# Kernel tuning notes

Hardware: AMD Instinct MI355X
Metric: run time of the kernel (lower is better)

Reference implementation:

```python
import jax, jax.numpy as jnp
import numpy as np

ALPHA = 0.2          # LeakyReLU negative slope
NEG_INF = -9e15      # mask value from the torch code
B, N, F, E, H, S, T, L = 32, 128, 78, 12, 256, 20, 13, 3


def setup_inputs() -> dict:
    key = jax.random.key(0)
    ks = jax.random.split(key, 20)
    sc = 0.05  # param scale
    inp = {
        "node_features": jax.random.normal(ks[0], (B, N, F), jnp.float32),
        "edge_features": jax.random.normal(ks[1], (B, N, N, E), jnp.float32),
        "adj_matrix": jax.random.randint(ks[2], (B, N, N), 0, 2).astype(jnp.int32),
        "scaffold_features": jax.random.normal(ks[3], (B, S), jnp.float32),
        # node projection (Linear F->H, with bias)
        "W_node": jax.random.normal(ks[4], (F, H), jnp.float32) * sc,
        "b_node": jnp.zeros((H,), jnp.float32),
        # stacked GAT layer params: W (H->H, no bias), a (2H->1, no bias)
        "gat_W": jax.random.normal(ks[5], (L, H, H), jnp.float32) * sc,
        "gat_a": jax.random.normal(ks[6], (L, 2 * H), jnp.float32) * sc,
        # scaffold projection (S->H)
        "W_sc": jax.random.normal(ks[7], (S, H), jnp.float32) * sc,
        "b_sc": jnp.zeros((H,), jnp.float32),
        # graph_pooling MLP: H -> H/2 -> H/4 (shared for graph + scaffold paths)
        "gp_w1": jax.random.normal(ks[8], (H, H // 2), jnp.float32) * sc,
        "gp_b1": jnp.zeros((H // 2,), jnp.float32),
        "gp_w2": jax.random.normal(ks[9], (H // 2, H // 4), jnp.float32) * sc,
        "gp_b2": jnp.zeros((H // 4,), jnp.float32),
        # output MLP: (H/4 + H/4) -> H/2 -> T
        "out_w1": jax.random.normal(ks[10], (H // 2, H // 2), jnp.float32) * sc,
        "out_b1": jnp.zeros((H // 2,), jnp.float32),
        "out_w2": jax.random.normal(ks[11], (H // 2, T), jnp.float32) * sc,
        "out_b2": jnp.zeros((T,), jnp.float32),
    }
    return inp


def _gat_stack(x, adj_matrix, gat_W, gat_a):
    # x: (B,N,H); adj: (B,N,N) int
    mask = adj_matrix > 0
    n_layers, _, h_dim = gat_W.shape
    for l in range(n_layers):
        h = jnp.einsum("bnf,fh->bnh", x, gat_W[l])      # (B,N,H)
        a1, a2 = gat_a[l, :h_dim], gat_a[l, h_dim:]
        # a . [h_i ; h_j] == h_i.a1 + h_j.a2 (exact decomposition of the
        # O(N^2, 2H) concat in the torch code)
        s1 = h @ a1                                       # (B,N)
        s2 = h @ a2                                       # (B,N)
        e = jax.nn.leaky_relu(s1[:, :, None] + s2[:, None, :], ALPHA)
        att = jnp.where(mask, e, NEG_INF)                 # (B,N,N)
        att = jax.nn.softmax(att, axis=-1)
        h_prime = jnp.einsum("bij,bjh->bih", att, h)
        x = jax.nn.relu(h_prime)                          # relu after layer (dropout = identity, eval)
    return x


def _pool(z, gp_w1, gp_b1, gp_w2, gp_b2):
    z = jax.nn.relu(z @ gp_w1 + gp_b1)
    return jax.nn.relu(z @ gp_w2 + gp_b2)


def reference(node_features, edge_features, adj_matrix, scaffold_features,
              W_node, b_node, gat_W, gat_a, W_sc, b_sc,
              gp_w1, gp_b1, gp_w2, gp_b2, out_w1, out_b1, out_w2, out_b2):
    # edge_features is accepted but unused in the original forward
    x = node_features @ W_node + b_node                  # (B,N,H)
    x = _gat_stack(x, adj_matrix, gat_W, gat_a)
    graph = x.mean(axis=1)                               # (B,H)
    g = _pool(graph, gp_w1, gp_b1, gp_w2, gp_b2)         # (B,H/4)
    s = _pool(scaffold_features @ W_sc + b_sc, gp_w1, gp_b1, gp_w2, gp_b2)
    c = jnp.concatenate([g, s], axis=-1)                 # (B,H/2)
    hdn = jax.nn.relu(c @ out_w1 + out_b1)
    return hdn @ out_w2 + out_b2                         # (B,T)
```

## Files before the change

### kernel.cpp

```cpp
#include <hip/hip_runtime.h>
#include <hip/hip_bf16.h>

#define NEG_INF -9.0e15f

using u16 = unsigned short;

__device__ __forceinline__ float b2f(__hip_bfloat16 v) { return __bfloat162float(v); }
__device__ __forceinline__ float ldv(const float* p, int i) { return p[i]; }
__device__ __forceinline__ float ldv(const __hip_bfloat16* p, int i) { return __bfloat162float(p[i]); }

__device__ __forceinline__ void async16(const void* g, void* l) {
    __builtin_amdgcn_global_load_lds(
        (__attribute__((address_space(1))) void*)(g),
        (__attribute__((address_space(3))) void*)(l), 16, 0, 0);
}

__device__ __forceinline__ int sniff(const void* wnode) {
    const u16* w = (const u16*)wnode;
    int lane = threadIdx.x & 63;
    u16 u = w[2 * lane];
    int e = (u >> 7) & 0xFF;
    unsigned long long m = __ballot(e >= 100 && e <= 140);
    return __popcll(m) >= 48;
}


template <int IS_BF>
__device__ __forceinline__ void gat_core(
    char* smem, int t, int row0, int pb0,
    const void* __restrict__ gat_W, const void* __restrict__ gat_a, int l,
    float* __restrict__ hw, float* __restrict__ s1w, float* __restrict__ s2w) {
    float* xsT = (float*)smem;
    const int tx = t & 63, w = t >> 6;
    const int c0 = 4 * tx;
    float acc0[4], acc1[4];
    #pragma unroll
    for (int j = 0; j < 4; ++j) { acc0[j] = 0.f; acc1[j] = 0.f; }

    if (IS_BF) {
        u16* Wb0 = (u16*)(smem + 10240);
        const u16* Wl = (const u16*)gat_W + (size_t)l * 65536;
        auto stage_rows = [&](int r0, int nr, int buf) {
            const char* g = (const char*)Wl + (size_t)r0 * 512;
            char* lp = (char*)(Wb0 + buf * 8192);
            int bytes = nr * 512;
            for (int off = t * 16; off < bytes; off += 4096)
                async16(g + off, lp + off);
        };
        int pb = pb0;
        for (int tt = 0; tt < 8; ++tt) {
            if (tt < 7) stage_rows(32 * (tt + 1), 32, pb ^ 1);
            const u16* Wp = Wb0 + pb * 8192;
            const int k0 = 32 * tt;
            #pragma unroll 8
            for (int kk = 0; kk < 32; ++kk) {
                uint2 wv = *(const uint2*)(Wp + kk * 256 + c0);
                float w0 = __uint_as_float(wv.x << 16);
                float w1 = __uint_as_float(wv.x & 0xffff0000u);
                float w2 = __uint_as_float(wv.y << 16);
                float w3 = __uint_as_float(wv.y & 0xffff0000u);
                float2 xp = *(const float2*)&xsT[(k0 + kk) * 10 + 2 * w];
                acc0[0] += xp.x * w0; acc0[1] += xp.x * w1;
                acc0[2] += xp.x * w2; acc0[3] += xp.x * w3;
                acc1[0] += xp.y * w0; acc1[1] += xp.y * w1;
                acc1[2] += xp.y * w2; acc1[3] += xp.y * w3;
            }
            __syncthreads();
            pb ^= 1;
        }
        const __hip_bfloat16* ga = (const __hip_bfloat16*)gat_a + (size_t)l * 512;
        float d10 = 0.f, d20 = 0.f, d11 = 0.f, d21 = 0.f;
        #pragma unroll
        for (int j = 0; j < 4; ++j) {
            float a1v = b2f(ga[c0 + j]), a2v = b2f(ga[256 + c0 + j]);
            d10 += acc0[j] * a1v; d20 += acc0[j] * a2v;
            d11 += acc1[j] * a1v; d21 += acc1[j] * a2v;
        }
        #pragma unroll
        for (int off = 1; off < 64; off <<= 1) {
            d10 += __shfl_xor(d10, off, 64); d20 += __shfl_xor(d20, off, 64);
            d11 += __shfl_xor(d11, off, 64); d21 += __shfl_xor(d21, off, 64);
        }
        if (tx == 0) {
            s1w[row0 + 2 * w] = d10;     s2w[row0 + 2 * w] = d20;
            s1w[row0 + 2 * w + 1] = d11; s2w[row0 + 2 * w + 1] = d21;
        }
        *(float4*)&hw[(size_t)(row0 + 2 * w) * 256 + c0]     = (float4){acc0[0], acc0[1], acc0[2], acc0[3]};
        *(float4*)&hw[(size_t)(row0 + 2 * w + 1) * 256 + c0] = (float4){acc1[0], acc1[1], acc1[2], acc1[3]};
    } else {
        const float* Wlf = (const float*)gat_W + (size_t)l * 65536;
        const float* gaf = (const float*)gat_a + (size_t)l * 512;
        #pragma unroll 4
        for (int k = 0; k < 256; ++k) {
            float4 wf = *(const float4*)(Wlf + k * 256 + c0);
            float2 xp = *(const float2*)&xsT[k * 10 + 2 * w];
            acc0[0] += xp.x * wf.x; acc0[1] += xp.x * wf.y;
            acc0[2] += xp.x * wf.z; acc0[3] += xp.x * wf.w;
            acc1[0] += xp.y * wf.x; acc1[1] += xp.y * wf.y;
            acc1[2] += xp.y * wf.z; acc1[3] += xp.y * wf.w;
        }
        float d10 = 0.f, d20 = 0.f, d11 = 0.f, d21 = 0.f;
        #pragma unroll
        for (int j = 0; j < 4; ++j) {
            float a1v = gaf[c0 + j], a2v = gaf[256 + c0 + j];
            d10 += acc0[j] * a1v; d20 += acc0[j] * a2v;
            d11 += acc1[j] * a1v; d21 += acc1[j] * a2v;
        }
        #pragma unroll
        for (int off = 1; off < 64; off <<= 1) {
            d10 += __shfl_xor(d10, off, 64); d20 += __shfl_xor(d20, off, 64);
            d11 += __shfl_xor(d11, off, 64); d21 += __shfl_xor(d21, off, 64);
        }
        if (tx == 0) {
            s1w[row0 + 2 * w] = d10;     s2w[row0 + 2 * w] = d20;
            s1w[row0 + 2 * w + 1] = d11; s2w[row0 + 2 * w + 1] = d21;
        }
        *(float4*)&hw[(size_t)(row0 + 2 * w) * 256 + c0]     = (float4){acc0[0], acc0[1], acc0[2], acc0[3]};
        *(float4*)&hw[(size_t)(row0 + 2 * w + 1) * 256 + c0] = (float4){acc1[0], acc1[1], acc1[2], acc1[3]};
    }
}

__device__ __forceinline__ void attn_compute(
    char* smem, int t, int b, int s,
    const float* __restrict__ hw, const float* __restrict__ s1w,
    const float* __restrict__ s2w, const int* __restrict__ adj,
    float ac0[4], float ac1[4]) {
    float (*att_t)[10] = (float (*)[10])smem;
    float* hbuf = (float*)(smem + 5120);
    const int i0 = s << 3;
    const int w = t >> 6, lane = t & 63;
    const char* hbytes = (const char*)(hw + (size_t)b * 32768);
    const int ph = s & 3;
    {
        char* lb = (char*)hbuf;
        const char* g = hbytes + ph * 32768;
        #pragma unroll
        for (int i = 0; i < 8; ++i)
            async16(g + i * 4096 + t * 16, lb + i * 4096 + t * 16);
    }
    {
        int cc0 = lane, cc1 = lane + 64;
        int ir0 = i0 + 2 * w, ir1 = ir0 + 1;
        const int* a0 = adj + (size_t)(b * 128 + ir0) * 128;
        const int* a1 = adj + (size_t)(b * 128 + ir1) * 128;
        int m00 = a0[cc0], m01 = a0[cc1], m10 = a1[cc0], m11 = a1[cc1];
        float sv0 = s1w[b * 128 + ir0], sv1 = s1w[b * 128 + ir1];
        float t0 = s2w[b * 128 + cc0],  t1 = s2w[b * 128 + cc1];
        float e00 = sv0 + t0; e00 = (e00 >= 0.f) ? e00 : 0.2f * e00;
        float e01 = sv0 + t1; e01 = (e01 >= 0.f) ? e01 : 0.2f * e01;
        float e10 = sv1 + t0; e10 = (e10 >= 0.f) ? e10 : 0.2f * e10;
        float e11 = sv1 + t1; e11 = (e11 >= 0.f) ? e11 : 0.2f * e11;
        float v00 = (m00 > 0) ? e00 : NEG_INF;
        float v01 = (m01 > 0) ? e01 : NEG_INF;
        float v10 = (m10 > 0) ? e10 : NEG_INF;
        float v11 = (m11 > 0) ? e11 : NEG_INF;
        float mx0 = fmaxf(v00, v01), mx1 = fmaxf(v10, v11);
        #pragma unroll
        for (int off = 1; off < 64; off <<= 1) {
            mx0 = fmaxf(mx0, __shfl_xor(mx0, off, 64));
            mx1 = fmaxf(mx1, __shfl_xor(mx1, off, 64));
        }
        float p00 = __expf(v00 - mx0), p01 = __expf(v01 - mx0);
        float p10 = __expf(v10 - mx1), p11 = __expf(v11 - mx1);
        float sm0 = p00 + p01, sm1 = p10 + p11;
        #pragma unroll
        for (int off = 1; off < 64; off <<= 1) {
            sm0 += __shfl_xor(sm0, off, 64);
            sm1 += __shfl_xor(sm1, off, 64);
        }
        float inv0 = 1.0f / sm0, inv1 = 1.0f / sm1;
        att_t[cc0][2 * w]     = p00 * inv0;
        att_t[cc1][2 * w]     = p01 * inv0;
        att_t[cc0][2 * w + 1] = p10 * inv1;
        att_t[cc1][2 * w + 1] = p11 * inv1;
    }
    __syncthreads();
    int tx = t & 63, ty = t >> 6;
    #pragma unroll
    for (int j = 0; j < 4; ++j) { ac0[j] = 0.f; ac1[j] = 0.f; }
    for (int c = 0; c < 4; ++c) {
        if (c < 3) {
            char* lb = (char*)hbuf + ((c + 1) & 1) * 32768;
            const char* g = hbytes + (((c + 1 + ph) & 3) * 32768);
            #pragma unroll
            for (int i = 0; i < 8; ++i)
                async16(g + i * 4096 + t * 16, lb + i * 4096 + t * 16);
        }
        const float* hc = hbuf + (c & 1) * 8192;
        const int jb = ((c + ph) & 3) * 32;
        #pragma unroll 4
        for (int jj = 0; jj < 32; ++jj) {
            float4 hv = *(const float4*)&hc[jj * 256 + 4 * tx];
            float2 ap = *(const float2*)&att_t[jb + jj][2 * ty];
            ac0[0] += ap.x * hv.x; ac0[1] += ap.x * hv.y;
            ac0[2] += ap.x * hv.z; ac0[3] += ap.x * hv.w;
            ac1[0] += ap.y * hv.x; ac1[1] += ap.y * hv.y;
            ac1[2] += ap.y * hv.z; ac1[3] += ap.y * hv.w;
        }
        __syncthreads();
    }
}

__global__ __launch_bounds__(256) void k_gat_first(
    const void* __restrict__ nf, const void* __restrict__ Wn_raw,
    const void* __restrict__ bn,
    const void* __restrict__ gat_W, const void* __restrict__ gat_a,
    float* __restrict__ hw, float* __restrict__ s1w, float* __restrict__ s2w) {
    __shared__ __align__(16) char smem[43008];
    const int t = threadIdx.x;
    const int row0 = blockIdx.x * 8;
    const int tx = t & 63, w = t >> 6;
    const int c0 = 4 * tx;
    float* xsT = (float*)smem;
    float acc0[4], acc1[4];

    if (sniff(Wn_raw)) {
        u16* Wb0 = (u16*)(smem + 10240);
        const u16* Wl = (const u16*)gat_W;
        auto stage = [&](const u16* src, int r0, int nr, int buf) {
            const char* g = (const char*)src + (size_t)r0 * 512;
            char* lp = (char*)(Wb0 + buf * 8192);
            int bytes = nr * 512;
            for (int off = t * 16; off < bytes; off += 4096)
                async16(g + off, lp + off);
        };
        auto tile = [&](int buf, int k0, int nr) {
            const u16* Wp = Wb0 + buf * 8192;
            #pragma unroll 8
            for (int kk = 0; kk < nr; ++kk) {
                uint2 wv = *(const uint2*)(Wp + kk * 256 + c0);
                float w0 = __uint_as_float(wv.x << 16);
                float w1 = __uint_as_float(wv.x & 0xffff0000u);
                float w2 = __uint_as_float(wv.y << 16);
                float w3 = __uint_as_float(wv.y & 0xffff0000u);
                float2 xp = *(const float2*)&xsT[(k0 + kk) * 10 + 2 * w];
                acc0[0] += xp.x * w0; acc0[1] += xp.x * w1;
                acc0[2] += xp.x * w2; acc0[3] += xp.x * w3;
                acc1[0] += xp.y * w0; acc1[1] += xp.y * w1;
                acc1[2] += xp.y * w2; acc1[3] += xp.y * w3;
            }
        };
        const u16* Wnl = (const u16*)Wn_raw;
        stage(Wnl, 0, 32, 0);
        const u16* nfu = (const u16*)nf;
        for (int i = t; i < 624; i += 256) {
            int r = i / 78, k = i - r * 78;
            xsT[k * 10 + r] = __uint_as_float(((unsigned)nfu[(row0 + r) * 78 + k]) << 16);
        }
        const __hip_bfloat16* bnb = (const __hip_bfloat16*)bn;
        #pragma unroll
        for (int j = 0; j < 4; ++j) { acc0[j] = b2f(bnb[c0 + j]); acc1[j] = acc0[j]; }
        __syncthreads();
        stage(Wnl, 32, 32, 1);
        tile(0, 0, 32);
        __syncthreads();
        stage(Wnl, 64, 14, 0);
        tile(1, 32, 32);
        __syncthreads();
        stage(Wl, 0, 32, 1);
        tile(0, 64, 14);
        __syncthreads();
        #pragma unroll
        for (int j = 0; j < 4; ++j) {
            xsT[(c0 + j) * 10 + 2 * w]     = acc0[j];
            xsT[(c0 + j) * 10 + 2 * w + 1] = acc1[j];
        }
        __syncthreads();
        gat_core<1>(smem, t, row0, 1, gat_W, gat_a, 0, hw, s1w, s2w);
    } else {
        const float* nff = (const float*)nf;
        for (int i = t; i < 624; i += 256) {
            int r = i / 78, k = i - r * 78;
            xsT[k * 10 + r] = nff[(row0 + r) * 78 + k];
        }
        __syncthreads();
        const float* Wnf = (const float*)Wn_raw;
        const float* bnf = (const float*)bn;
        #pragma unroll
        for (int j = 0; j < 4; ++j) { acc0[j] = bnf[c0 + j]; acc1[j] = acc0[j]; }
        for (int k = 0; k < 78; ++k) {
            float4 wf = *(const float4*)(Wnf + k * 256 + c0);
            float2 xp = *(const float2*)&xsT[k * 10 + 2 * w];
            acc0[0] += xp.x * wf.x; acc0[1] += xp.x * wf.y;
            acc0[2] += xp.x * wf.z; acc0[3] += xp.x * wf.w;
            acc1[0] += xp.y * wf.x; acc1[1] += xp.y * wf.y;
            acc1[2] += xp.y * wf.z; acc1[3] += xp.y * wf.w;
        }
        __syncthreads();
        #pragma unroll
        for (int j = 0; j < 4; ++j) {
            xsT[(c0 + j) * 10 + 2 * w]     = acc0[j];
            xsT[(c0 + j) * 10 + 2 * w + 1] = acc1[j];
        }
        __syncthreads();
        gat_core<0>(smem, t, row0, 0, gat_W, gat_a, 0, hw, s1w, s2w);
    }
}

__global__ __launch_bounds__(256) void k_attn_gat(
    const float* __restrict__ h_in, const float* __restrict__ s1_in,
    const float* __restrict__ s2_in, const int* __restrict__ adj,
    const void* __restrict__ gat_W, const void* __restrict__ gat_a, int l,
    const void* __restrict__ Wn_raw,
    float* __restrict__ h_out, float* __restrict__ s1_out, float* __restrict__ s2_out) {
    __shared__ __align__(16) char smem[74752];
    const int t = threadIdx.x;
    const int blk = blockIdx.x;
    const int b = blk >> 4, s = blk & 15;
    const int row0 = blk * 8;
    const int isbf = sniff(Wn_raw);

    float ac0[4], ac1[4];
    attn_compute(smem, t, b, s, h_in, s1_in, s2_in, adj, ac0, ac1);
    const int tx = t & 63, ty = t >> 6;
    const int c0 = 4 * tx;
    float* xsT = (float*)smem;
    if (isbf) {
        u16* Wb0 = (u16*)(smem + 10240);
        const u16* Wl = (const u16*)gat_W + (size_t)l * 65536;
        for (int off = t * 16; off < 16384; off += 4096)
            async16((const char*)Wl + off, (char*)Wb0 + off);
    }
    #pragma unroll
    for (int j = 0; j < 4; ++j) {
        xsT[(c0 + j) * 10 + 2 * ty]     = fmaxf(ac0[j], 0.f);
        xsT[(c0 + j) * 10 + 2 * ty + 1] = fmaxf(ac1[j], 0.f);
    }
    __syncthreads();
    if (isbf)
        gat_core<1>(smem, t, row0, 0, gat_W, gat_a, l, h_out, s1_out, s2_out);
    else
        gat_core<0>(smem, t, row0, 0, gat_W, gat_a, l, h_out, s1_out, s2_out);
}

__global__ __launch_bounds__(256) void k_attn_pool(
    const float* __restrict__ h_in, const float* __restrict__ s1_in,
    const float* __restrict__ s2_in, const int* __restrict__ adj,
    float* __restrict__ gpart) {
    __shared__ __align__(16) char smem[74752];
    const int t = threadIdx.x;
    const int blk = blockIdx.x;
    const int b = blk >> 4, s = blk & 15;
    float ac0[4], ac1[4];
    attn_compute(smem, t, b, s, h_in, s1_in, s2_in, adj, ac0, ac1);
    float (*pool_red)[256] = (float (*)[256])(smem + 70656);
    const int tx = t & 63, ty = t >> 6;
    float4 pr = {(fmaxf(ac0[0],0.f) + fmaxf(ac1[0],0.f)) * (1.f/128.f),
                 (fmaxf(ac0[1],0.f) + fmaxf(ac1[1],0.f)) * (1.f/128.f),
                 (fmaxf(ac0[2],0.f) + fmaxf(ac1[2],0.f)) * (1.f/128.f),
                 (fmaxf(ac0[3],0.f) + fmaxf(ac1[3],0.f)) * (1.f/128.f)};
    *(float4*)&pool_red[ty][4 * tx] = pr;
    __syncthreads();
    if (t < 64) {
        float4 r0 = ((const float4*)&pool_red[0][0])[t];
        float4 r1 = ((const float4*)&pool_red[1][0])[t];
        float4 r2 = ((const float4*)&pool_red[2][0])[t];
        float4 r3 = ((const float4*)&pool_red[3][0])[t];
        float4 o = {r0.x+r1.x+r2.x+r3.x, r0.y+r1.y+r2.y+r3.y,
                    r0.z+r1.z+r2.z+r3.z, r0.w+r1.w+r2.w+r3.w};
        *(float4*)&gpart[((size_t)b * 16 + s) * 256 + 4 * t] = o;
    }
}

template <typename T>
__device__ __forceinline__ void head_body(
    int b, int t, const float* __restrict__ gpart,
    const T* scaf, const T* W_sc, const T* b_sc,
    const T* gp_w1, const T* gp_b1, const T* gp_w2, const T* gp_b2,
    const T* out_w1, const T* out_b1, const T* out_w2, const T* out_b2,
    float* gin_s, float* sproj, float* scaf_s,
    float* red1, float* red2, float* z1g, float* z1s,
    float* cvec, float* hdn, float* outv) {
    float g = 0.f;
    #pragma unroll
    for (int gg = 0; gg < 16; ++gg) g += gpart[((size_t)b * 16 + gg) * 256 + t];
    gin_s[t] = g;
    if (t < 20) scaf_s[t] = ldv(scaf, b * 20 + t);
    __syncthreads();
    {
        float sa = ldv(b_sc, t);
        #pragma unroll
        for (int k = 0; k < 20; ++k) sa += scaf_s[k] * ldv(W_sc, k * 256 + t);
        sproj[t] = sa;
    }
    __syncthreads();
    {
        int j = t & 127, khalf = t >> 7;
        int k0 = khalf * 128;
        float a1 = 0.f, a2 = 0.f;
        #pragma unroll 16
        for (int kk = 0; kk < 128; ++kk) {
            int k = k0 + kk;
            float wv = ldv(gp_w1, k * 128 + j);
            a1 += gin_s[k] * wv;
            a2 += sproj[k] * wv;
        }
        red1[t] = a1; red2[t] = a2;
    }
    __syncthreads();
    if (t < 128) {
        float bb = ldv(gp_b1, t);
        z1g[t] = fmaxf(bb + red1[t] + red1[t + 128], 0.f);
        z1s[t] = fmaxf(bb + red2[t] + red2[t + 128], 0.f);
    }
    __syncthreads();
    {
        int j = t & 63, q = t >> 6;
        int k0 = q * 32;
        float a1 = 0.f, a2 = 0.f;
        #pragma unroll
        for (int kk = 0; kk < 32; ++kk) {
            int k = k0 + kk;
            float wv = ldv(gp_w2, k * 64 + j);
            a1 += z1g[k] * wv;
            a2 += z1s[k] * wv;
        }
        red1[t] = a1; red2[t] = a2;
    }
    __syncthreads();
    if (t < 64) {
        float bb = ldv(gp_b2, t);
        cvec[t]      = fmaxf(bb + red1[t] + red1[t + 64] + red1[t + 128] + red1[t + 192], 0.f);
        cvec[64 + t] = fmaxf(bb + red2[t] + red2[t + 64] + red2[t + 128] + red2[t + 192], 0.f);
    }
    __syncthreads();
    {
        int j = t & 127, khalf = t >> 7;
        int k0 = khalf * 64;
        float a = 0.f;
        #pragma unroll 16
        for (int kk = 0; kk < 64; ++kk) {
            int k = k0 + kk;
            a += cvec[k] * ldv(out_w1, k * 128 + j);
        }
        red1[t] = a;
    }
    __syncthreads();
    if (t < 128) hdn[t] = fmaxf(ldv(out_b1, t) + red1[t] + red1[t + 128], 0.f);
    __syncthreads();
    if (t < 13) {
        float a = ldv(out_b2, t);
        #pragma unroll 16
        for (int k = 0; k < 128; ++k) a += hdn[k] * ldv(out_w2, k * 13 + t);
        outv[t] = a;
    }
}

__global__ __launch_bounds__(256) void k_head(
    const float* __restrict__ gpart, const void* __restrict__ scaf,
    const void* __restrict__ W_sc, const void* __restrict__ b_sc,
    const void* __restrict__ gp_w1, const void* __restrict__ gp_b1,
    const void* __restrict__ gp_w2, const void* __restrict__ gp_b2,
    const void* __restrict__ out_w1, const void* __restrict__ out_b1,
    const void* __restrict__ out_w2, const void* __restrict__ out_b2,
    void* __restrict__ out, const void* __restrict__ Wn) {
    int isbf = sniff(Wn);
    int b = blockIdx.x;
    int t = threadIdx.x;
    __shared__ float gin_s[256], sproj[256], scaf_s[20];
    __shared__ float red1[256], red2[256];
    __shared__ float z1g[128], z1s[128], cvec[128], hdn[128], outv[13];
    if (isbf) {
        head_body<__hip_bfloat16>(b, t, gpart,
            (const __hip_bfloat16*)scaf, (const __hip_bfloat16*)W_sc, (const __hip_bfloat16*)b_sc,
            (const __hip_bfloat16*)gp_w1, (const __hip_bfloat16*)gp_b1,
            (const __hip_bfloat16*)gp_w2, (const __hip_bfloat16*)gp_b2,
            (const __hip_bfloat16*)out_w1, (const __hip_bfloat16*)out_b1,
            (const __hip_bfloat16*)out_w2, (const __hip_bfloat16*)out_b2,
            gin_s, sproj, scaf_s, red1, red2, z1g, z1s, cvec, hdn, outv);
    } else {
        head_body<float>(b, t, gpart,
            (const float*)scaf, (const float*)W_sc, (const float*)b_sc,
            (const float*)gp_w1, (const float*)gp_b1,
            (const float*)gp_w2, (const float*)gp_b2,
            (const float*)out_w1, (const float*)out_b1,
            (const float*)out_w2, (const float*)out_b2,
            gin_s, sproj, scaf_s, red1, red2, z1g, z1s, cvec, hdn, outv);
    }
    __syncthreads();
    if (t < 13) {
        if (isbf) ((__hip_bfloat16*)out)[b * 13 + t] = __float2bfloat16(outv[t]);
        else      ((float*)out)[b * 13 + t] = outv[t];
    }
}

extern "C" void kernel_launch(void* const* d_in, const int* in_sizes, int n_in,
                              void* d_out, int out_size, void* d_ws, size_t ws_size,
                              hipStream_t stream) {
    (void)in_sizes; (void)n_in; (void)out_size; (void)ws_size;
    const void* nf     = d_in[0];
    const int*  adj    = (const int*)d_in[2];
    const void* scaf   = d_in[3];
    const void* W_node = d_in[4];
    const void* b_node = d_in[5];
    const void* gat_W  = d_in[6];
    const void* gat_a  = d_in[7];
    const void* W_sc   = d_in[8];
    const void* b_sc   = d_in[9];
    const void* gp_w1  = d_in[10];
    const void* gp_b1  = d_in[11];
    const void* gp_w2  = d_in[12];
    const void* gp_b2  = d_in[13];
    const void* out_w1 = d_in[14];
    const void* out_b1 = d_in[15];
    const void* out_w2 = d_in[16];
    const void* out_b2 = d_in[17];

    float* ws    = (float*)d_ws;
    float* hA    = ws;
    float* hB    = ws + 1048576;
    float* s1A   = ws + 2097152;
    float* s2A   = ws + 2101248;
    float* s1B   = ws + 2105344;
    float* s2B   = ws + 2109440;
    float* gpart = ws + 2113536;

    k_gat_first<<<512, 256, 0, stream>>>(nf, W_node, b_node, gat_W, gat_a,
                                         hA, s1A, s2A);
    k_attn_gat<<<512, 256, 0, stream>>>(hA, s1A, s2A, adj, gat_W, gat_a, 1,
                                        W_node, hB, s1B, s2B);
    k_attn_gat<<<512, 256, 0, stream>>>(hB, s1B, s2B, adj, gat_W, gat_a, 2,
                                        W_node, hA, s1A, s2A);
    k_attn_pool<<<512, 256, 0, stream>>>(hA, s1A, s2A, adj, gpart);
    k_head<<<32, 256, 0, stream>>>(gpart, scaf, W_sc, b_sc, gp_w1, gp_b1, gp_w2, gp_b2,
                                   out_w1, out_b1, out_w2, out_b2, d_out, W_node);
}
```

Measured before the change: 205.0 us.

## Halve rows per block to double grid size and raise occupancy

Each block now handles 4 node rows instead of 8, one per wave, so every kernel launches 1024 blocks instead of 512. Shared memory per block roughly halves, and launch bounds request 4 blocks per CU, aiming for better latency hiding and fuller use of the CUs. The trade-off is that each block reloads the full weight matrix and the per-graph h tiles for half as many rows, which doubles that global and LDS traffic per useful output. The head kernel now reduces 32 partial sums per graph instead of 16.

```diff
diff --git a/kernel.cpp b/kernel.cpp
--- a/kernel.cpp
+++ b/kernel.cpp
@@ -33,16 +33,14 @@
     float* xsT = (float*)smem;
     const int tx = t & 63, w = t >> 6;
     const int c0 = 4 * tx;
-    float acc0[4], acc1[4];
-    #pragma unroll
-    for (int j = 0; j < 4; ++j) { acc0[j] = 0.f; acc1[j] = 0.f; }
+    float acc[4] = {0.f, 0.f, 0.f, 0.f};
 
     if (IS_BF) {
-        u16* Wb0 = (u16*)(smem + 10240);
+        u16* Wb0 = (u16*)(smem + 5120);
         const u16* Wl = (const u16*)gat_W + (size_t)l * 65536;
         auto stage_rows = [&](int r0, int nr, int buf) {
             const char* g = (const char*)Wl + (size_t)r0 * 512;
-            char* lp = (char*)(Wb0 + buf * 8192);
+            char* lp = (char*)Wb0 + buf * 16384;
             int bytes = nr * 512;
             for (int off = t * 16; off < bytes; off += 4096)
                 async16(g + off, lp + off);
@@ -59,64 +57,50 @@
                 float w1 = __uint_as_float(wv.x & 0xffff0000u);
                 float w2 = __uint_as_float(wv.y << 16);
                 float w3 = __uint_as_float(wv.y & 0xffff0000u);
-                float2 xp = *(const float2*)&xsT[(k0 + kk) * 10 + 2 * w];
-                acc0[0] += xp.x * w0; acc0[1] += xp.x * w1;
-                acc0[2] += xp.x * w2; acc0[3] += xp.x * w3;
-                acc1[0] += xp.y * w0; acc1[1] += xp.y * w1;
-                acc1[2] += xp.y * w2; acc1[3] += xp.y * w3;
+                float xv = xsT[(k0 + kk) * 5 + w];
+                acc[0] += xv * w0; acc[1] += xv * w1;
+                acc[2] += xv * w2; acc[3] += xv * w3;
             }
             __syncthreads();
             pb ^= 1;
         }
         const __hip_bfloat16* ga = (const __hip_bfloat16*)gat_a + (size_t)l * 512;
-        float d10 = 0.f, d20 = 0.f, d11 = 0.f, d21 = 0.f;
+        float d1 = 0.f, d2 = 0.f;
         #pragma unroll
         for (int j = 0; j < 4; ++j) {
-            float a1v = b2f(ga[c0 + j]), a2v = b2f(ga[256 + c0 + j]);
-            d10 += acc0[j] * a1v; d20 += acc0[j] * a2v;
-            d11 += acc1[j] * a1v; d21 += acc1[j] * a2v;
+            d1 += acc[j] * b2f(ga[c0 + j]);
+            d2 += acc[j] * b2f(ga[256 + c0 + j]);
         }
         #pragma unroll
         for (int off = 1; off < 64; off <<= 1) {
-            d10 += __shfl_xor(d10, off, 64); d20 += __shfl_xor(d20, off, 64);
-            d11 += __shfl_xor(d11, off, 64); d21 += __shfl_xor(d21, off, 64);
-        }
-        if (tx == 0) {
-            s1w[row0 + 2 * w] = d10;     s2w[row0 + 2 * w] = d20;
-            s1w[row0 + 2 * w + 1] = d11; s2w[row0 + 2 * w + 1] = d21;
-        }
-        *(float4*)&hw[(size_t)(row0 + 2 * w) * 256 + c0]     = (float4){acc0[0], acc0[1], acc0[2], acc0[3]};
-        *(float4*)&hw[(size_t)(row0 + 2 * w + 1) * 256 + c0] = (float4){acc1[0], acc1[1], acc1[2], acc1[3]};
+            d1 += __shfl_xor(d1, off, 64);
+            d2 += __shfl_xor(d2, off, 64);
+        }
+        if (tx == 0) { s1w[row0 + w] = d1; s2w[row0 + w] = d2; }
+        *(float4*)&hw[(size_t)(row0 + w) * 256 + c0] = (float4){acc[0], acc[1], acc[2], acc[3]};
     } else {
         const float* Wlf = (const float*)gat_W + (size_t)l * 65536;
         const float* gaf = (const float*)gat_a + (size_t)l * 512;
         #pragma unroll 4
         for (int k = 0; k < 256; ++k) {
             float4 wf = *(const float4*)(Wlf + k * 256 + c0);
-            float2 xp = *(const float2*)&xsT[k * 10 + 2 * w];
-            acc0[0] += xp.x * wf.x; acc0[1] += xp.x * wf.y;
-            acc0[2] += xp.x * wf.z; acc0[3] += xp.x * wf.w;
-            acc1[0] += xp.y * wf.x; acc1[1] += xp.y * wf.y;
-            acc1[2] += xp.y * wf.z; acc1[3] += xp.y * wf.w;
-        }
-        float d10 = 0.f, d20 = 0.f, d11 = 0.f, d21 = 0.f;
+            float xv = xsT[k * 5 + w];
+            acc[0] += xv * wf.x; acc[1] += xv * wf.y;
+            acc[2] += xv * wf.z; acc[3] += xv * wf.w;
+        }
+        float d1 = 0.f, d2 = 0.f;
         #pragma unroll
         for (int j = 0; j < 4; ++j) {
-            float a1v = gaf[c0 + j], a2v = gaf[256 + c0 + j];
-            d10 += acc0[j] * a1v; d20 += acc0[j] * a2v;
-            d11 += acc1[j] * a1v; d21 += acc1[j] * a2v;
+            d1 += acc[j] * gaf[c0 + j];
+            d2 += acc[j] * gaf[256 + c0 + j];
         }
         #pragma unroll
         for (int off = 1; off < 64; off <<= 1) {
-            d10 += __shfl_xor(d10, off, 64); d20 += __shfl_xor(d20, off, 64);
-            d11 += __shfl_xor(d11, off, 64); d21 += __shfl_xor(d21, off, 64);
-        }
-        if (tx == 0) {
-            s1w[row0 + 2 * w] = d10;     s2w[row0 + 2 * w] = d20;
-            s1w[row0 + 2 * w + 1] = d11; s2w[row0 + 2 * w + 1] = d21;
-        }
-        *(float4*)&hw[(size_t)(row0 + 2 * w) * 256 + c0]     = (float4){acc0[0], acc0[1], acc0[2], acc0[3]};
-        *(float4*)&hw[(size_t)(row0 + 2 * w + 1) * 256 + c0] = (float4){acc1[0], acc1[1], acc1[2], acc1[3]};
+            d1 += __shfl_xor(d1, off, 64);
+            d2 += __shfl_xor(d2, off, 64);
+        }
+        if (tx == 0) { s1w[row0 + w] = d1; s2w[row0 + w] = d2; }
+        *(float4*)&hw[(size_t)(row0 + w) * 256 + c0] = (float4){acc[0], acc[1], acc[2], acc[3]};
     }
 }
 
@@ -124,102 +108,88 @@
     char* smem, int t, int b, int s,
     const float* __restrict__ hw, const float* __restrict__ s1w,
     const float* __restrict__ s2w, const int* __restrict__ adj,
-    float ac0[4], float ac1[4]) {
-    float (*att_t)[10] = (float (*)[10])smem;
-    float* hbuf = (float*)(smem + 5120);
-    const int i0 = s << 3;
+    float ac[4]) {
+    float (*att_t)[6] = (float (*)[6])smem;
+    float* hbuf = (float*)(smem + 3072);
+    const int i0 = s << 2;
     const int w = t >> 6, lane = t & 63;
     const char* hbytes = (const char*)(hw + (size_t)b * 32768);
-    const int ph = s & 3;
+    const int ph = s & 7;
     {
         char* lb = (char*)hbuf;
-        const char* g = hbytes + ph * 32768;
-        #pragma unroll
-        for (int i = 0; i < 8; ++i)
+        const char* g = hbytes + ph * 16384;
+        #pragma unroll
+        for (int i = 0; i < 4; ++i)
             async16(g + i * 4096 + t * 16, lb + i * 4096 + t * 16);
     }
     {
         int cc0 = lane, cc1 = lane + 64;
-        int ir0 = i0 + 2 * w, ir1 = ir0 + 1;
-        const int* a0 = adj + (size_t)(b * 128 + ir0) * 128;
-        const int* a1 = adj + (size_t)(b * 128 + ir1) * 128;
-        int m00 = a0[cc0], m01 = a0[cc1], m10 = a1[cc0], m11 = a1[cc1];
-        float sv0 = s1w[b * 128 + ir0], sv1 = s1w[b * 128 + ir1];
-        float t0 = s2w[b * 128 + cc0],  t1 = s2w[b * 128 + cc1];
-        float e00 = sv0 + t0; e00 = (e00 >= 0.f) ? e00 : 0.2f * e00;
-        float e01 = sv0 + t1; e01 = (e01 >= 0.f) ? e01 : 0.2f * e01;
-        float e10 = sv1 + t0; e10 = (e10 >= 0.f) ? e10 : 0.2f * e10;
-        float e11 = sv1 + t1; e11 = (e11 >= 0.f) ? e11 : 0.2f * e11;
-        float v00 = (m00 > 0) ? e00 : NEG_INF;
-        float v01 = (m01 > 0) ? e01 : NEG_INF;
-        float v10 = (m10 > 0) ? e10 : NEG_INF;
-        float v11 = (m11 > 0) ? e11 : NEG_INF;
-        float mx0 = fmaxf(v00, v01), mx1 = fmaxf(v10, v11);
-        #pragma unroll
-        for (int off = 1; off < 64; off <<= 1) {
-            mx0 = fmaxf(mx0, __shfl_xor(mx0, off, 64));
-            mx1 = fmaxf(mx1, __shfl_xor(mx1, off, 64));
-        }
-        float p00 = __expf(v00 - mx0), p01 = __expf(v01 - mx0);
-        float p10 = __expf(v10 - mx1), p11 = __expf(v11 - mx1);
-        float sm0 = p00 + p01, sm1 = p10 + p11;
-        #pragma unroll
-        for (int off = 1; off < 64; off <<= 1) {
-            sm0 += __shfl_xor(sm0, off, 64);
-            sm1 += __shfl_xor(sm1, off, 64);
-        }
-        float inv0 = 1.0f / sm0, inv1 = 1.0f / sm1;
-        att_t[cc0][2 * w]     = p00 * inv0;
-        att_t[cc1][2 * w]     = p01 * inv0;
-        att_t[cc0][2 * w + 1] = p10 * inv1;
-        att_t[cc1][2 * w + 1] = p11 * inv1;
-    }
-    __syncthreads();
-    int tx = t & 63, ty = t >> 6;
-    #pragma unroll
-    for (int j = 0; j < 4; ++j) { ac0[j] = 0.f; ac1[j] = 0.f; }
-    for (int c = 0; c < 4; ++c) {
-        if (c < 3) {
-            char* lb = (char*)hbuf + ((c + 1) & 1) * 32768;
-            const char* g = hbytes + (((c + 1 + ph) & 3) * 32768);
+        int ir = i0 + w;
+        const int* a0 = adj + (size_t)(b * 128 + ir) * 128;
+        int m0 = a0[cc0], m1 = a0[cc1];
+        float sv = s1w[b * 128 + ir];
+        float t0 = s2w[b * 128 + cc0], t1 = s2w[b * 128 + cc1];
+        float e0 = sv + t0; e0 = (e0 >= 0.f) ? e0 : 0.2f * e0;
+        float e1 = sv + t1; e1 = (e1 >= 0.f) ? e1 : 0.2f * e1;
+        float v0 = (m0 > 0) ? e0 : NEG_INF;
+        float v1 = (m1 > 0) ? e1 : NEG_INF;
+        float mx = fmaxf(v0, v1);
+        #pragma unroll
+        for (int off = 1; off < 64; off <<= 1)
+            mx = fmaxf(mx, __shfl_xor(mx, off, 64));
+        float p0 = __expf(v0 - mx), p1 = __expf(v1 - mx);
+        float sm = p0 + p1;
+        #pragma unroll
+        for (int off = 1; off < 64; off <<= 1)
+            sm += __shfl_xor(sm, off, 64);
+        float inv = 1.0f / sm;
+        att_t[cc0][w] = p0 * inv;
+        att_t[cc1][w] = p1 * inv;
+    }
+    __syncthreads();
+    const int tx = t & 63;
+    const int c0 = 4 * tx;
+    ac[0] = 0.f; ac[1] = 0.f; ac[2] = 0.f; ac[3] = 0.f;
+    for (int c = 0; c < 8; ++c) {
+        if (c < 7) {
+            char* lb = (char*)hbuf + ((c + 1) & 1) * 16384;
+            const char* g = hbytes + (((c + 1 + ph) & 7) * 16384);
             #pragma unroll
-            for (int i = 0; i < 8; ++i)
+            for (int i = 0; i < 4; ++i)
                 async16(g + i * 4096 + t * 16, lb + i * 4096 + t * 16);
         }
-        const float* hc = hbuf + (c & 1) * 8192;
-        const int jb = ((c + ph) & 3) * 32;
+        const float* hc = hbuf + (c & 1) * 4096;
+        const int jb = ((c + ph) & 7) * 16;
         #pragma unroll 4
-        for (int jj = 0; jj < 32; ++jj) {
-            float4 hv = *(const float4*)&hc[jj * 256 + 4 * tx];
-            float2 ap = *(const float2*)&att_t[jb + jj][2 * ty];
-            ac0[0] += ap.x * hv.x; ac0[1] += ap.x * hv.y;
-            ac0[2] += ap.x * hv.z; ac0[3] += ap.x * hv.w;
-            ac1[0] += ap.y * hv.x; ac1[1] += ap.y * hv.y;
-            ac1[2] += ap.y * hv.z; ac1[3] += ap.y * hv.w;
-        }
-        __syncthreads();
-    }
-}
-
-__global__ __launch_bounds__(256) void k_gat_first(
+        for (int jj = 0; jj < 16; ++jj) {
+            float4 hv = *(const float4*)&hc[jj * 256 + c0];
+            float ap = att_t[jb + jj][w];
+            ac[0] += ap * hv.x; ac[1] += ap * hv.y;
+            ac[2] += ap * hv.z; ac[3] += ap * hv.w;
+        }
+        __syncthreads();
+    }
+}
+
+__global__ __launch_bounds__(256, 4) void k_gat_first(
     const void* __restrict__ nf, const void* __restrict__ Wn_raw,
     const void* __restrict__ bn,
     const void* __restrict__ gat_W, const void* __restrict__ gat_a,
     float* __restrict__ hw, float* __restrict__ s1w, float* __restrict__ s2w) {
-    __shared__ __align__(16) char smem[43008];
+    __shared__ __align__(16) char smem[37888];
     const int t = threadIdx.x;
-    const int row0 = blockIdx.x * 8;
+    const int row0 = blockIdx.x * 4;
     const int tx = t & 63, w = t >> 6;
     const int c0 = 4 * tx;
     float* xsT = (float*)smem;
-    float acc0[4], acc1[4];
+    float acc[4];
 
     if (sniff(Wn_raw)) {
-        u16* Wb0 = (u16*)(smem + 10240);
+        u16* Wb0 = (u16*)(smem + 5120);
         const u16* Wl = (const u16*)gat_W;
         auto stage = [&](const u16* src, int r0, int nr, int buf) {
             const char* g = (const char*)src + (size_t)r0 * 512;
-            char* lp = (char*)(Wb0 + buf * 8192);
+            char* lp = (char*)Wb0 + buf * 16384;
             int bytes = nr * 512;
             for (int off = t * 16; off < bytes; off += 4096)
                 async16(g + off, lp + off);
@@ -233,23 +203,21 @@
                 float w1 = __uint_as_float(wv.x & 0xffff0000u);
                 float w2 = __uint_as_float(wv.y << 16);
                 float w3 = __uint_as_float(wv.y & 0xffff0000u);
-                float2 xp = *(const float2*)&xsT[(k0 + kk) * 10 + 2 * w];
-                acc0[0] += xp.x * w0; acc0[1] += xp.x * w1;
-                acc0[2] += xp.x * w2; acc0[3] += xp.x * w3;
-                acc1[0] += xp.y * w0; acc1[1] += xp.y * w1;
-                acc1[2] += xp.y * w2; acc1[3] += xp.y * w3;
+                float xv = xsT[(k0 + kk) * 5 + w];
+                acc[0] += xv * w0; acc[1] += xv * w1;
+                acc[2] += xv * w2; acc[3] += xv * w3;
             }
         };
         const u16* Wnl = (const u16*)Wn_raw;
         stage(Wnl, 0, 32, 0);
         const u16* nfu = (const u16*)nf;
-        for (int i = t; i < 624; i += 256) {
+        for (int i = t; i < 312; i += 256) {
             int r = i / 78, k = i - r * 78;
-            xsT[k * 10 + r] = __uint_as_float(((unsigned)nfu[(row0 + r) * 78 + k]) << 16);
+            xsT[k * 5 + r] = __uint_as_float(((unsigned)nfu[(row0 + r) * 78 + k]) << 16);
         }
         const __hip_bfloat16* bnb = (const __hip_bfloat16*)bn;
         #pragma unroll
-        for (int j = 0; j < 4; ++j) { acc0[j] = b2f(bnb[c0 + j]); acc1[j] = acc0[j]; }
+        for (int j = 0; j < 4; ++j) acc[j] = b2f(bnb[c0 + j]);
         __syncthreads();
         stage(Wnl, 32, 32, 1);
         tile(0, 0, 32);
@@ -261,71 +229,61 @@
         tile(0, 64, 14);
         __syncthreads();
         #pragma unroll
-        for (int j = 0; j < 4; ++j) {
-            xsT[(c0 + j) * 10 + 2 * w]     = acc0[j];
-            xsT[(c0 + j) * 10 + 2 * w + 1] = acc1[j];
-        }
+        for (int j = 0; j < 4; ++j) xsT[(c0 + j) * 5 + w] = acc[j];
         __syncthreads();
         gat_core<1>(smem, t, row0, 1, gat_W, gat_a, 0, hw, s1w, s2w);
     } else {
         const float* nff = (const float*)nf;
-        for (int i = t; i < 624; i += 256) {
+        for (int i = t; i < 312; i += 256) {
             int r = i / 78, k = i - r * 78;
-            xsT[k * 10 + r] = nff[(row0 + r) * 78 + k];
+            xsT[k * 5 + r] = nff[(row0 + r) * 78 + k];
         }
         __syncthreads();
         const float* Wnf = (const float*)Wn_raw;
         const float* bnf = (const float*)bn;
         #pragma unroll
-        for (int j = 0; j < 4; ++j) { acc0[j] = bnf[c0 + j]; acc1[j] = acc0[j]; }
+        for (int j = 0; j < 4; ++j) acc[j] = bnf[c0 + j];
         for (int k = 0; k < 78; ++k) {
             float4 wf = *(const float4*)(Wnf + k * 256 + c0);
-            float2 xp = *(const float2*)&xsT[k * 10 + 2 * w];
-            acc0[0] += xp.x * wf.x; acc0[1] += xp.x * wf.y;
-            acc0[2] += xp.x * wf.z; acc0[3] += xp.x * wf.w;
-            acc1[0] += xp.y * wf.x; acc1[1] += xp.y * wf.y;
-            acc1[2] += xp.y * wf.z; acc1[3] += xp.y * wf.w;
-        }
-        __syncthreads();
-        #pragma unroll
-        for (int j = 0; j < 4; ++j) {
-            xsT[(c0 + j) * 10 + 2 * w]     = acc0[j];
-            xsT[(c0 + j) * 10 + 2 * w + 1] = acc1[j];
-        }
+            float xv = xsT[k * 5 + w];
+            acc[0] += xv * wf.x; acc[1] += xv * wf.y;
+            acc[2] += xv * wf.z; acc[3] += xv * wf.w;
+        }
+        __syncthreads();
+        #pragma unroll
+        for (int j = 0; j < 4; ++j) xsT[(c0 + j) * 5 + w] = acc[j];
         __syncthreads();
         gat_core<0>(smem, t, row0, 0, gat_W, gat_a, 0, hw, s1w, s2w);
     }
 }
 
-__global__ __launch_bounds__(256) void k_attn_gat(
+__global__ __launch_bounds__(256, 4) void k_attn_gat(
     const float* __restrict__ h_in, const float* __restrict__ s1_in,
     const float* __restrict__ s2_in, const int* __restrict__ adj,
     const void* __restrict__ gat_W, const void* __restrict__ gat_a, int l,
     const void* __restrict__ Wn_raw,
     float* __restrict__ h_out, float* __restrict__ s1_out, float* __restrict__ s2_out) {
-    __shared__ __align__(16) char smem[74752];
+    __shared__ __align__(16) char smem[37888];
     const int t = threadIdx.x;
     const int blk = blockIdx.x;
-    const int b = blk >> 4, s = blk & 15;
-    const int row0 = blk * 8;
+    const int b = blk >> 5, s = blk & 31;
+    const int row0 = blk * 4;
     const int isbf = sniff(Wn_raw);
 
-    float ac0[4], ac1[4];
-    attn_compute(smem, t, b, s, h_in, s1_in, s2_in, adj, ac0, ac1);
-    const int tx = t & 63, ty = t >> 6;
+    float ac[4];
+    attn_compute(smem, t, b, s, h_in, s1_in, s2_in, adj, ac);
+    const int tx = t & 63, w = t >> 6;
     const int c0 = 4 * tx;
     float* xsT = (float*)smem;
     if (isbf) {
-        u16* Wb0 = (u16*)(smem + 10240);
+        u16* Wb0 = (u16*)(smem + 5120);
         const u16* Wl = (const u16*)gat_W + (size_t)l * 65536;
         for (int off = t * 16; off < 16384; off += 4096)
             async16((const char*)Wl + off, (char*)Wb0 + off);
     }
     #pragma unroll
-    for (int j = 0; j < 4; ++j) {
-        xsT[(c0 + j) * 10 + 2 * ty]     = fmaxf(ac0[j], 0.f);
-        xsT[(c0 + j) * 10 + 2 * ty + 1] = fmaxf(ac1[j], 0.f);
-    }
+    for (int j = 0; j < 4; ++j)
+        xsT[(c0 + j) * 5 + w] = fmaxf(ac[j], 0.f);
     __syncthreads();
     if (isbf)
         gat_core<1>(smem, t, row0, 0, gat_W, gat_a, l, h_out, s1_out, s2_out);
@@ -333,23 +291,21 @@
         gat_core<0>(smem, t, row0, 0, gat_W, gat_a, l, h_out, s1_out, s2_out);
 }
 
-__global__ __launch_bounds__(256) void k_attn_pool(
+__global__ __launch_bounds__(256, 4) void k_attn_pool(
     const float* __restrict__ h_in, const float* __restrict__ s1_in,
     const float* __restrict__ s2_in, const int* __restrict__ adj,
     float* __restrict__ gpart) {
-    __shared__ __align__(16) char smem[74752];
+    __shared__ __align__(16) char smem[39936];
     const int t = threadIdx.x;
     const int blk = blockIdx.x;
-    const int b = blk >> 4, s = blk & 15;
-    float ac0[4], ac1[4];
-    attn_compute(smem, t, b, s, h_in, s1_in, s2_in, adj, ac0, ac1);
-    float (*pool_red)[256] = (float (*)[256])(smem + 70656);
-    const int tx = t & 63, ty = t >> 6;
-    float4 pr = {(fmaxf(ac0[0],0.f) + fmaxf(ac1[0],0.f)) * (1.f/128.f),
-                 (fmaxf(ac0[1],0.f) + fmaxf(ac1[1],0.f)) * (1.f/128.f),
-                 (fmaxf(ac0[2],0.f) + fmaxf(ac1[2],0.f)) * (1.f/128.f),
-                 (fmaxf(ac0[3],0.f) + fmaxf(ac1[3],0.f)) * (1.f/128.f)};
-    *(float4*)&pool_red[ty][4 * tx] = pr;
+    const int b = blk >> 5, s = blk & 31;
+    float ac[4];
+    attn_compute(smem, t, b, s, h_in, s1_in, s2_in, adj, ac);
+    float (*pool_red)[256] = (float (*)[256])(smem + 35840);
+    const int tx = t & 63, w = t >> 6;
+    float4 pr = {fmaxf(ac[0], 0.f) * (1.f/128.f), fmaxf(ac[1], 0.f) * (1.f/128.f),
+                 fmaxf(ac[2], 0.f) * (1.f/128.f), fmaxf(ac[3], 0.f) * (1.f/128.f)};
+    *(float4*)&pool_red[w][4 * tx] = pr;
     __syncthreads();
     if (t < 64) {
         float4 r0 = ((const float4*)&pool_red[0][0])[t];
@@ -358,7 +314,7 @@
         float4 r3 = ((const float4*)&pool_red[3][0])[t];
         float4 o = {r0.x+r1.x+r2.x+r3.x, r0.y+r1.y+r2.y+r3.y,
                     r0.z+r1.z+r2.z+r3.z, r0.w+r1.w+r2.w+r3.w};
-        *(float4*)&gpart[((size_t)b * 16 + s) * 256 + 4 * t] = o;
+        *(float4*)&gpart[((size_t)b * 32 + s) * 256 + 4 * t] = o;
     }
 }
 
@@ -373,7 +329,7 @@
     float* cvec, float* hdn, float* outv) {
     float g = 0.f;
     #pragma unroll
-    for (int gg = 0; gg < 16; ++gg) g += gpart[((size_t)b * 16 + gg) * 256 + t];
+    for (int gg = 0; gg < 32; ++gg) g += gpart[((size_t)b * 32 + gg) * 256 + t];
     gin_s[t] = g;
     if (t < 20) scaf_s[t] = ldv(scaf, b * 20 + t);
     __syncthreads();
@@ -515,13 +471,13 @@
     float* s2B   = ws + 2109440;
     float* gpart = ws + 2113536;
 
-    k_gat_first<<<512, 256, 0, stream>>>(nf, W_node, b_node, gat_W, gat_a,
-                                         hA, s1A, s2A);
-    k_attn_gat<<<512, 256, 0, stream>>>(hA, s1A, s2A, adj, gat_W, gat_a, 1,
-                                        W_node, hB, s1B, s2B);
-    k_attn_gat<<<512, 256, 0, stream>>>(hB, s1B, s2B, adj, gat_W, gat_a, 2,
-                                        W_node, hA, s1A, s2A);
-    k_attn_pool<<<512, 256, 0, stream>>>(hA, s1A, s2A, adj, gpart);
+    k_gat_first<<<1024, 256, 0, stream>>>(nf, W_node, b_node, gat_W, gat_a,
+                                          hA, s1A, s2A);
+    k_attn_gat<<<1024, 256, 0, stream>>>(hA, s1A, s2A, adj, gat_W, gat_a, 1,
+                                         W_node, hB, s1B, s2B);
+    k_attn_gat<<<1024, 256, 0, stream>>>(hB, s1B, s2B, adj, gat_W, gat_a, 2,
+                                         W_node, hA, s1A, s2A);
+    k_attn_pool<<<1024, 256, 0, stream>>>(hA, s1A, s2A, adj, gpart);
     k_head<<<32, 256, 0, stream>>>(gpart, scaf, W_sc, b_sc, gp_w1, gp_b1, gp_w2, gp_b2,
                                    out_w1, out_b1, out_w2, out_b2, d_out, W_node);
 }
```

New measurement: 246.2 us. +20.1%, slower.
